# Kernel optimization log

Measured on AMD Instinct MI355X. Metric: run time of the kernel, lower is better.

## Reference

```python
import jax, jax.numpy as jnp
import numpy as np

K = 2  # top-k experts selected per token (config['k'])
SPARSITY_EPS = 1e-05


def setup_inputs() -> dict:
    key = jax.random.key(0)
    k1, k2, k3 = jax.random.split(key, 3)
    N, D, E = 8192, 768, 16  # tokens, hidden dim, num experts
    f = jax.random.normal(k1, (N, D, E), dtype=jnp.float32)   # stacked expert outputs
    x = jax.random.normal(k2, (N, D), dtype=jnp.float32)      # routing inputs
    W = jax.random.normal(k3, (E, D), dtype=jnp.float32) * 0.02  # gate Linear weight
    b = jnp.zeros((E,), dtype=jnp.float32)                    # gate Linear bias
    return {"f": f, "x": x, "W": W, "b": b}


def reference(f, x, W, b):
    # gate logits: [N, E]
    gate_logits = x @ W.T + b
    N, E = gate_logits.shape

    # top-k selection + softmax over selected logits.
    # scatter(-inf) then softmax over the full expert axis is mathematically
    # identical to softmax over the k selected values scattered back to zeros.
    vals, idx = jax.lax.top_k(gate_logits, K)          # [N, K], [N, K]
    w = jax.nn.softmax(vals, axis=-1)                  # [N, K]
    rows = jnp.arange(N)[:, None]                      # [N, 1]
    g = jnp.zeros((N, E), gate_logits.dtype).at[rows, idx].set(w)[..., None]  # [N, E, 1]

    # batched expert combine: [N, D, E] @ [N, E, 1] -> [N, D]
    y = jnp.matmul(f, g)[..., 0]

    # metrics (the ones returned by the torch forward)
    s_concat = jnp.where(g < SPARSITY_EPS, 1.0, 0.0).astype(g.dtype)  # [N, E, 1]
    soft_averages = jnp.mean(g, axis=0)                               # [E, 1]
    hard_averages = jnp.mean(1.0 - s_concat, axis=0)                  # [E, 1]

    return (y, soft_averages, hard_averages, s_concat, 0)
```

## Files before the change

kernel.cpp:

```cpp
#include <hip/hip_runtime.h>
#include <math.h>

#define N_TOK 8192
#define DDIM  768
#define NEXP  16

#define SOFT_OFF (N_TOK*DDIM)
#define HARD_OFF (SOFT_OFF + NEXP)
#define S_OFF    (HARD_OFF + NEXP)
#define SCAL_OFF (S_OFF + N_TOK*NEXP)

extern "C" __global__ void init_out_kernel(float* __restrict__ out) {
  int t = threadIdx.x;
  if (t < 2*NEXP) out[SOFT_OFF + t] = 0.0f;
  if (t == 0) out[SCAL_OFF] = 0.0f;
}

__device__ __forceinline__ void fma4(float4& a, float s, float4 w) {
  a.x = fmaf(s, w.x, a.x);
  a.y = fmaf(s, w.y, a.y);
  a.z = fmaf(s, w.z, a.z);
  a.w = fmaf(s, w.w, a.w);
}

__device__ __forceinline__ void xred(float& v) {
  v += __shfl_xor(v, 4);
  v += __shfl_xor(v, 8);
  v += __shfl_xor(v, 16);
  v += __shfl_xor(v, 32);
}

__device__ __forceinline__ void finish_token(
    int n, float4 av, int lane, float* __restrict__ out,
    float4* __restrict__ table, float* s_soft, float* s_hard) {
  float v[16];
  #pragma unroll
  for (int q = 0; q < 4; ++q) {
    v[q*4+0] = __shfl(av.x, q);
    v[q*4+1] = __shfl(av.y, q);
    v[q*4+2] = __shfl(av.z, q);
    v[q*4+3] = __shfl(av.w, q);
  }
  float v0 = -INFINITY, v1 = -INFINITY;
  int e0 = 0, e1 = 0;
  #pragma unroll
  for (int j = 0; j < 16; ++j) {
    float val = v[j];
    if (val > v0) { v1 = v0; e1 = e0; v0 = val; e0 = j; }
    else if (val > v1) { v1 = val; e1 = j; }
  }
  float t1 = expf(v1 - v0);
  float inv = 1.0f / (1.0f + t1);
  float w0 = inv;
  float w1 = t1 * inv;
  if (lane == 0) {
    table[n] = make_float4(__int_as_float(e0), __int_as_float(e1), w0, w1);
  }
  if (lane < NEXP) {
    float g = (lane == e0) ? w0 : ((lane == e1) ? w1 : 0.0f);
    bool sel = (g >= 1e-5f);
    out[S_OFF + (size_t)n*NEXP + lane] = sel ? 0.0f : 1.0f;
    atomicAdd(&s_soft[lane], g);
    if (sel) atomicAdd(&s_hard[lane], 1.0f);
  }
}

extern "C" __global__ __launch_bounds__(256) void gate_kernel(
    const float* __restrict__ x, const float* __restrict__ W,
    const float* __restrict__ bias, float* __restrict__ out,
    float4* __restrict__ table) {
  __shared__ float Wl[DDIM*NEXP];
  __shared__ float s_soft[NEXP];
  __shared__ float s_hard[NEXP];
  int tid = threadIdx.x;
  if (tid < NEXP) { s_soft[tid] = 0.0f; s_hard[tid] = 0.0f; }
  for (int idx = tid; idx < DDIM*NEXP; idx += 256) {
    int d = idx >> 4, e = idx & 15;
    Wl[idx] = W[e*DDIM + d];
  }
  __syncthreads();

  int wave = tid >> 6;
  int lane = tid & 63;
  int e4 = lane & 3;
  int c  = lane >> 2;
  float4 bq = ((const float4*)bias)[e4];

  #pragma unroll
  for (int p = 0; p < 2; ++p) {
    int pairi = (blockIdx.x*4 + wave) + p*2048;
    int n0 = pairi*2, n1 = n0 + 1;
    const float* x0p = x + (size_t)n0*DDIM + c*48;
    const float* x1p = x + (size_t)n1*DDIM + c*48;
    const float* wbase = &Wl[c*48*16 + 4*e4];
    float4 a0 = make_float4(0.f,0.f,0.f,0.f);
    float4 a1 = make_float4(0.f,0.f,0.f,0.f);
    #pragma unroll
    for (int m = 0; m < 12; ++m) {
      float4 xv0 = *(const float4*)(x0p + 4*m);
      float4 xv1 = *(const float4*)(x1p + 4*m);
      const float* wb = wbase + m*64;
      float4 wq0 = *(const float4*)(wb);
      float4 wq1 = *(const float4*)(wb + 16);
      float4 wq2 = *(const float4*)(wb + 32);
      float4 wq3 = *(const float4*)(wb + 48);
      fma4(a0, xv0.x, wq0); fma4(a0, xv0.y, wq1);
      fma4(a0, xv0.z, wq2); fma4(a0, xv0.w, wq3);
      fma4(a1, xv1.x, wq0); fma4(a1, xv1.y, wq1);
      fma4(a1, xv1.z, wq2); fma4(a1, xv1.w, wq3);
    }
    xred(a0.x); xred(a0.y); xred(a0.z); xred(a0.w);
    xred(a1.x); xred(a1.y); xred(a1.z); xred(a1.w);
    a0.x += bq.x; a0.y += bq.y; a0.z += bq.z; a0.w += bq.w;
    a1.x += bq.x; a1.y += bq.y; a1.z += bq.z; a1.w += bq.w;
    finish_token(n0, a0, lane, out, table, s_soft, s_hard);
    finish_token(n1, a1, lane, out, table, s_soft, s_hard);
  }
  __syncthreads();
  if (tid < NEXP) {
    atomicAdd(&out[SOFT_OFF + tid], s_soft[tid] * (1.0f/N_TOK));
    atomicAdd(&out[HARD_OFF + tid], s_hard[tid] * (1.0f/N_TOK));
  }
}

extern "C" __global__ __launch_bounds__(256) void combine_kernel(
    const float* __restrict__ f, const float4* __restrict__ table,
    float* __restrict__ y) {
  int n = blockIdx.x;
  float4 rec = table[n];
  int e0 = __float_as_int(rec.x);
  int e1 = __float_as_int(rec.y);
  float w0 = rec.z, w1 = rec.w;
  int tid = threadIdx.x;
  int jg = (tid & 3) * 4;
  float4 gq;
  gq.x = (jg+0 == e0) ? w0 : ((jg+0 == e1) ? w1 : 0.0f);
  gq.y = (jg+1 == e0) ? w0 : ((jg+1 == e1) ? w1 : 0.0f);
  gq.z = (jg+2 == e0) ? w0 : ((jg+2 == e1) ? w1 : 0.0f);
  gq.w = (jg+3 == e0) ? w0 : ((jg+3 == e1) ? w1 : 0.0f);
  const float4* fp = (const float4*)(f + (size_t)n * (DDIM*NEXP));
  float* yr = y + (size_t)n * DDIM;
  #pragma unroll
  for (int k = 0; k < 12; ++k) {
    int q = tid + 256*k;
    float4 v = fp[q];
    float part = v.x*gq.x + v.y*gq.y + v.z*gq.z + v.w*gq.w;
    part += __shfl_xor(part, 1);
    part += __shfl_xor(part, 2);
    if ((tid & 3) == 0) yr[q >> 2] = part;
  }
}

extern "C" void kernel_launch(void* const* d_in, const int* in_sizes, int n_in,
                              void* d_out, int out_size, void* d_ws, size_t ws_size,
                              hipStream_t stream) {
  const float* f = (const float*)d_in[0];
  const float* x = (const float*)d_in[1];
  const float* W = (const float*)d_in[2];
  const float* b = (const float*)d_in[3];
  float* out = (float*)d_out;
  float4* table = (float4*)d_ws;

  hipLaunchKernelGGL(init_out_kernel, dim3(1), dim3(64), 0, stream, out);
  hipLaunchKernelGGL(gate_kernel, dim3(512), dim3(256), 0, stream,
                     x, W, b, out, table);
  hipLaunchKernelGGL(combine_kernel, dim3(N_TOK), dim3(256), 0, stream,
                     f, table, out );
}
```

Baseline: 116.7 us.

## Fuse gating and expert combine into one per-token kernel with nontemporal f loads

Replaces the separate gate and combine kernels with a single kernel where each block computes its token's gate logits, top-2 softmax and metrics, then combines the expert outputs. This removes the intermediate routing table round trip and one dependent launch. Global atomics per token go to a workspace and are scaled in a small finalize kernel. In exchange, W is re-read from global/L2 by every block and there are more global atomics (up to 4 per token) contending on 32 addresses. The f stream now uses nontemporal loads and y uses nontemporal stores.

```diff
diff --git a/kernel.cpp b/kernel.cpp
--- a/kernel.cpp
+++ b/kernel.cpp
@@ -5,149 +5,103 @@
 #define DDIM  768
 #define NEXP  16
 
+typedef float f32x4 __attribute__((ext_vector_type(4)));
+
 #define SOFT_OFF (N_TOK*DDIM)
 #define HARD_OFF (SOFT_OFF + NEXP)
 #define S_OFF    (HARD_OFF + NEXP)
 #define SCAL_OFF (S_OFF + N_TOK*NEXP)
 
-extern "C" __global__ void init_out_kernel(float* __restrict__ out) {
+extern "C" __global__ void init_ws_kernel(float* __restrict__ ws) {
   int t = threadIdx.x;
-  if (t < 2*NEXP) out[SOFT_OFF + t] = 0.0f;
+  if (t < 2*NEXP) ws[t] = 0.0f;
+}
+
+extern "C" __global__ void finalize_kernel(const float* __restrict__ ws,
+                                           float* __restrict__ out) {
+  int t = threadIdx.x;
+  if (t < 2*NEXP) out[SOFT_OFF + t] = ws[t] * (1.0f/N_TOK);
   if (t == 0) out[SCAL_OFF] = 0.0f;
 }
 
-__device__ __forceinline__ void fma4(float4& a, float s, float4 w) {
-  a.x = fmaf(s, w.x, a.x);
-  a.y = fmaf(s, w.y, a.y);
-  a.z = fmaf(s, w.z, a.z);
-  a.w = fmaf(s, w.w, a.w);
-}
+extern "C" __global__ __launch_bounds__(256) void fused_kernel(
+    const float* __restrict__ f, const float* __restrict__ x,
+    const float* __restrict__ W, const float* __restrict__ bias,
+    float* __restrict__ out, float* __restrict__ ws) {
+  const int n   = blockIdx.x;
+  const int tid = threadIdx.x;
+  __shared__ float xs[DDIM];
+  __shared__ float part[256];
+  __shared__ float lg[NEXP];
 
-__device__ __forceinline__ void xred(float& v) {
-  v += __shfl_xor(v, 4);
-  v += __shfl_xor(v, 8);
-  v += __shfl_xor(v, 16);
-  v += __shfl_xor(v, 32);
-}
+  if (tid < DDIM/4)
+    ((f32x4*)xs)[tid] = ((const f32x4*)(x + (size_t)n*DDIM))[tid];
+  __syncthreads();
 
-__device__ __forceinline__ void finish_token(
-    int n, float4 av, int lane, float* __restrict__ out,
-    float4* __restrict__ table, float* s_soft, float* s_hard) {
-  float v[16];
-  #pragma unroll
-  for (int q = 0; q < 4; ++q) {
-    v[q*4+0] = __shfl(av.x, q);
-    v[q*4+1] = __shfl(av.y, q);
-    v[q*4+2] = __shfl(av.z, q);
-    v[q*4+3] = __shfl(av.w, q);
+  {
+    const int e = tid & 15;
+    const int c = tid >> 4;
+    const f32x4* wrow = (const f32x4*)(W + e*DDIM + c*48);
+    const f32x4* xrow = (const f32x4*)(xs + c*48);
+    float acc = 0.f;
+    #pragma unroll
+    for (int j = 0; j < 12; ++j) {
+      f32x4 wv = wrow[j];
+      f32x4 xv = xrow[j];
+      acc = fmaf(xv.x, wv.x, acc); acc = fmaf(xv.y, wv.y, acc);
+      acc = fmaf(xv.z, wv.z, acc); acc = fmaf(xv.w, wv.w, acc);
+    }
+    part[tid] = acc;
   }
+  __syncthreads();
+  if (tid < NEXP) {
+    float s = bias[tid];
+    #pragma unroll
+    for (int c = 0; c < 16; ++c) s += part[c*16 + tid];
+    lg[tid] = s;
+  }
+  __syncthreads();
+
   float v0 = -INFINITY, v1 = -INFINITY;
   int e0 = 0, e1 = 0;
   #pragma unroll
-  for (int j = 0; j < 16; ++j) {
-    float val = v[j];
+  for (int j = 0; j < NEXP; ++j) {
+    float val = lg[j];
     if (val > v0) { v1 = v0; e1 = e0; v0 = val; e0 = j; }
     else if (val > v1) { v1 = val; e1 = j; }
   }
-  float t1 = expf(v1 - v0);
+  float t1  = expf(v1 - v0);
   float inv = 1.0f / (1.0f + t1);
-  float w0 = inv;
-  float w1 = t1 * inv;
-  if (lane == 0) {
-    table[n] = make_float4(__int_as_float(e0), __int_as_float(e1), w0, w1);
+  float w0  = inv;
+  float w1  = t1 * inv;
+
+  if (tid < NEXP) {
+    float g  = (tid == e0) ? w0 : ((tid == e1) ? w1 : 0.0f);
+    bool sel = (g >= 1e-5f);
+    out[S_OFF + (size_t)n*NEXP + tid] = sel ? 0.0f : 1.0f;
+    if (tid == e0 || tid == e1) {
+      atomicAdd(&ws[tid], g);
+      if (sel) atomicAdd(&ws[NEXP + tid], 1.0f);
+    }
   }
-  if (lane < NEXP) {
-    float g = (lane == e0) ? w0 : ((lane == e1) ? w1 : 0.0f);
-    bool sel = (g >= 1e-5f);
-    out[S_OFF + (size_t)n*NEXP + lane] = sel ? 0.0f : 1.0f;
-    atomicAdd(&s_soft[lane], g);
-    if (sel) atomicAdd(&s_hard[lane], 1.0f);
-  }
-}
 
-extern "C" __global__ __launch_bounds__(256) void gate_kernel(
-    const float* __restrict__ x, const float* __restrict__ W,
-    const float* __restrict__ bias, float* __restrict__ out,
-    float4* __restrict__ table) {
-  __shared__ float Wl[DDIM*NEXP];
-  __shared__ float s_soft[NEXP];
-  __shared__ float s_hard[NEXP];
-  int tid = threadIdx.x;
-  if (tid < NEXP) { s_soft[tid] = 0.0f; s_hard[tid] = 0.0f; }
-  for (int idx = tid; idx < DDIM*NEXP; idx += 256) {
-    int d = idx >> 4, e = idx & 15;
-    Wl[idx] = W[e*DDIM + d];
-  }
-  __syncthreads();
-
-  int wave = tid >> 6;
-  int lane = tid & 63;
-  int e4 = lane & 3;
-  int c  = lane >> 2;
-  float4 bq = ((const float4*)bias)[e4];
-
-  #pragma unroll
-  for (int p = 0; p < 2; ++p) {
-    int pairi = (blockIdx.x*4 + wave) + p*2048;
-    int n0 = pairi*2, n1 = n0 + 1;
-    const float* x0p = x + (size_t)n0*DDIM + c*48;
-    const float* x1p = x + (size_t)n1*DDIM + c*48;
-    const float* wbase = &Wl[c*48*16 + 4*e4];
-    float4 a0 = make_float4(0.f,0.f,0.f,0.f);
-    float4 a1 = make_float4(0.f,0.f,0.f,0.f);
-    #pragma unroll
-    for (int m = 0; m < 12; ++m) {
-      float4 xv0 = *(const float4*)(x0p + 4*m);
-      float4 xv1 = *(const float4*)(x1p + 4*m);
-      const float* wb = wbase + m*64;
-      float4 wq0 = *(const float4*)(wb);
-      float4 wq1 = *(const float4*)(wb + 16);
-      float4 wq2 = *(const float4*)(wb + 32);
-      float4 wq3 = *(const float4*)(wb + 48);
-      fma4(a0, xv0.x, wq0); fma4(a0, xv0.y, wq1);
-      fma4(a0, xv0.z, wq2); fma4(a0, xv0.w, wq3);
-      fma4(a1, xv1.x, wq0); fma4(a1, xv1.y, wq1);
-      fma4(a1, xv1.z, wq2); fma4(a1, xv1.w, wq3);
-    }
-    xred(a0.x); xred(a0.y); xred(a0.z); xred(a0.w);
-    xred(a1.x); xred(a1.y); xred(a1.z); xred(a1.w);
-    a0.x += bq.x; a0.y += bq.y; a0.z += bq.z; a0.w += bq.w;
-    a1.x += bq.x; a1.y += bq.y; a1.z += bq.z; a1.w += bq.w;
-    finish_token(n0, a0, lane, out, table, s_soft, s_hard);
-    finish_token(n1, a1, lane, out, table, s_soft, s_hard);
-  }
-  __syncthreads();
-  if (tid < NEXP) {
-    atomicAdd(&out[SOFT_OFF + tid], s_soft[tid] * (1.0f/N_TOK));
-    atomicAdd(&out[HARD_OFF + tid], s_hard[tid] * (1.0f/N_TOK));
-  }
-}
-
-extern "C" __global__ __launch_bounds__(256) void combine_kernel(
-    const float* __restrict__ f, const float4* __restrict__ table,
-    float* __restrict__ y) {
-  int n = blockIdx.x;
-  float4 rec = table[n];
-  int e0 = __float_as_int(rec.x);
-  int e1 = __float_as_int(rec.y);
-  float w0 = rec.z, w1 = rec.w;
-  int tid = threadIdx.x;
-  int jg = (tid & 3) * 4;
-  float4 gq;
-  gq.x = (jg+0 == e0) ? w0 : ((jg+0 == e1) ? w1 : 0.0f);
-  gq.y = (jg+1 == e0) ? w0 : ((jg+1 == e1) ? w1 : 0.0f);
-  gq.z = (jg+2 == e0) ? w0 : ((jg+2 == e1) ? w1 : 0.0f);
-  gq.w = (jg+3 == e0) ? w0 : ((jg+3 == e1) ? w1 : 0.0f);
-  const float4* fp = (const float4*)(f + (size_t)n * (DDIM*NEXP));
-  float* yr = y + (size_t)n * DDIM;
+  const int jg = (tid & 3) * 4;
+  float gx = (jg+0 == e0) ? w0 : ((jg+0 == e1) ? w1 : 0.0f);
+  float gy = (jg+1 == e0) ? w0 : ((jg+1 == e1) ? w1 : 0.0f);
+  float gz = (jg+2 == e0) ? w0 : ((jg+2 == e1) ? w1 : 0.0f);
+  float gw = (jg+3 == e0) ? w0 : ((jg+3 == e1) ? w1 : 0.0f);
+  const f32x4* fp = (const f32x4*)(f + (size_t)n * (DDIM*NEXP));
+  float* yr = out + (size_t)n * DDIM;
   #pragma unroll
   for (int k = 0; k < 12; ++k) {
     int q = tid + 256*k;
-    float4 v = fp[q];
-    float part = v.x*gq.x + v.y*gq.y + v.z*gq.z + v.w*gq.w;
-    part += __shfl_xor(part, 1);
-    part += __shfl_xor(part, 2);
-    if ((tid & 3) == 0) yr[q >> 2] = part;
+    f32x4 v = __builtin_nontemporal_load(fp + q);
+    float p = v.x*gx + v.y*gy + v.z*gz + v.w*gw;
+    p += __shfl_xor(p, 1);
+    p += __shfl_xor(p, 2);
+    if ((tid & 3) == 0) {
+      __builtin_nontemporal_store(p, yr + (q >> 2));
+    }
   }
 }
 
@@ -159,11 +113,10 @@
   const float* W = (const float*)d_in[2];
   const float* b = (const float*)d_in[3];
   float* out = (float*)d_out;
-  float4* table = (float4*)d_ws;
+  float* ws  = (float*)d_ws;
 
-  hipLaunchKernelGGL(init_out_kernel, dim3(1), dim3(64), 0, stream, out);
-  hipLaunchKernelGGL(gate_kernel, dim3(512), dim3(256), 0, stream,
-                     x, W, b, out, table);
-  hipLaunchKernelGGL(combine_kernel, dim3(N_TOK), dim3(256), 0, stream,
-                     f, table, out );
+  hipLaunchKernelGGL(init_ws_kernel, dim3(1), dim3(64), 0, stream, ws);
+  hipLaunchKernelGGL(fused_kernel, dim3(N_TOK), dim3(256), 0, stream,
+                     f, x, W, b, out, ws);
+  hipLaunchKernelGGL(finalize_kernel, dim3(1), dim3(64), 0, stream, ws, out);
 }
```

After: 146.5 us. 1.25x slower.
